# Kernel optimization log

Measured on AMD Instinct MI355X. Metric: run time of the kernel, lower is better.

## Reference

```python
import jax, jax.numpy as jnp
import numpy as np

B, S, D, H = 2, 2048, 1024, 16
HD = D // H
SCALE = HD ** -0.5
EPS = 1e-5


def setup_inputs() -> dict:
    key = jax.random.key(0)
    ks = jax.random.split(key, 12)
    s = 1.0 / np.sqrt(D)
    return {
        "query": jax.random.normal(ks[0], (B, S, D), jnp.float32),
        "key_": jax.random.normal(ks[1], (B, S, D), jnp.float32),
        "value": jax.random.normal(ks[2], (B, S, D), jnp.float32),
        "Wq": jax.random.normal(ks[3], (D, D), jnp.float32) * s,
        "bq": jnp.zeros((D,), jnp.float32),
        "Wk": jax.random.normal(ks[4], (D, D), jnp.float32) * s,
        "bk": jnp.zeros((D,), jnp.float32),
        "Wv": jax.random.normal(ks[5], (D, D), jnp.float32) * s,
        "bv": jnp.zeros((D,), jnp.float32),
        "Wo": jax.random.normal(ks[6], (D, D), jnp.float32) * s,
        "bo": jnp.zeros((D,), jnp.float32),
        "gamma": jnp.ones((D,), jnp.float32),
        "beta": jnp.zeros((D,), jnp.float32),
    }


def _split_heads(x):
    # [B,S,D] -> [B,H,S,HD]
    return x.reshape(B, S, H, HD).transpose(0, 2, 1, 3)


def reference(query, key_, value, Wq, bq, Wk, bk, Wv, bv, Wo, bo, gamma, beta):
    q = _split_heads(query @ Wq + bq)
    k = _split_heads(key_ @ Wk + bk)
    v = _split_heads(value @ Wv + bv)
    # [B,H,S,S] attention scores
    scores = jnp.einsum("bhqd,bhkd->bhqk", q, k) * SCALE
    probs = jax.nn.softmax(scores, axis=-1)  # dropout is identity in eval
    attn = jnp.einsum("bhqk,bhkd->bhqd", probs, v)
    attn = attn.transpose(0, 2, 1, 3).reshape(B, S, D)
    attn = attn @ Wo + bo
    # residual + LayerNorm
    x = query + attn
    mu = jnp.mean(x, axis=-1, keepdims=True)
    var = jnp.mean(jnp.square(x - mu), axis=-1, keepdims=True)
    out = (x - mu) * jax.lax.rsqrt(var + EPS) * gamma + beta
    return out
```

## Files before the change

### kernel.cpp

```cpp
#include <hip/hip_runtime.h>
#include <hip/hip_bf16.h>

#define DEVI __device__ __forceinline__

constexpr int Bb  = 2;
constexpr int Ss  = 2048;
constexpr int Dd  = 1024;
constexpr int Hh  = 16;
constexpr int HDh = 64;
constexpr int Mr  = Bb * Ss;
constexpr float kEps = 1e-5f;
constexpr float kQScale = 0.18033688011112043f;

typedef unsigned short u16;
typedef unsigned int   u32;
typedef u16 u16x8 __attribute__((ext_vector_type(8)));
typedef u16 u16x4 __attribute__((ext_vector_type(4)));
typedef __attribute__((ext_vector_type(8)))  short s16x8;
typedef __attribute__((ext_vector_type(16))) float f32x16;
typedef __attribute__((ext_vector_type(4)))  u32   u32x4;

DEVI float bf2f(u16 u) {
  return __builtin_bit_cast(float, ((unsigned int)u) << 16);
}
DEVI u16 f2bf(float f) {
  unsigned int x = __builtin_bit_cast(unsigned int, f);
  return (u16)((x + 0x7FFFu + ((x >> 16) & 1u)) >> 16);
}
DEVI u32 cvt_pk_bf16(float a, float b) {
  u32 r;
  asm("v_cvt_pk_bf16_f32 %0, %1, %2" : "=v"(r) : "v"(a), "v"(b));
  return r;
}
DEVI float vexp2(float x) {
  float r;
  asm("v_exp_f32 %0, %1" : "=v"(r) : "v"(x));
  return r;
}

DEVI void gload_lds16(const void* g, void* l) {
  __builtin_amdgcn_global_load_lds(
      (const __attribute__((address_space(1))) unsigned int*)(unsigned long long)(size_t)g,
      (__attribute__((address_space(3))) unsigned int*)(unsigned int)(size_t)l,
      16, 0, 0);
}


__global__ __launch_bounds__(256) void pack_a_fm(
    const float* __restrict__ X0, const float* __restrict__ X1,
    u16* __restrict__ Y0, u16* __restrict__ Y1) {
  __shared__ u16 Tl[64 * 64];
  const int t  = threadIdx.x;
  const int k0 = blockIdx.x * 64, r0 = blockIdx.y * 64;
  const float* X = blockIdx.z ? X1 : X0;
  u16*         Y = blockIdx.z ? Y1 : Y0;
#pragma unroll
  for (int i = 0; i < 4; ++i) {
    const int idx = t + i * 256;
    const int r = idx >> 4, c4 = (idx & 15) << 2;
    const float4 v = *(const float4*)(X + (size_t)(r0 + r) * 1024 + k0 + c4);
    u16x4 p;
    p[0] = f2bf(v.x); p[1] = f2bf(v.y); p[2] = f2bf(v.z); p[3] = f2bf(v.w);
    *(u16x4*)&Tl[r * 64 + (c4 ^ (8 * (r & 7)))] = p;
  }
  __syncthreads();
#pragma unroll
  for (int i = 0; i < 2; ++i) {
    const int slot = t + i * 256;
    const int f = slot >> 6, l = slot & 63;
    const int l31 = l & 31, g2 = l >> 5;
    const int r = (f >> 2) * 32 + l31;
    const int c = (f & 3) * 16 + g2 * 8;
    const u16x8 v = *(const u16x8*)&Tl[r * 64 + (c ^ (8 * (r & 7)))];
    const size_t t32 = (size_t)(r0 >> 5) + (f >> 2);
    const int s = (k0 >> 4) + (f & 3);
    *(u16x8*)(Y + (t32 * 64 + s) * 512 + l * 8) = v;
  }
}

__global__ __launch_bounds__(256) void pack_w_fm(
    const float* __restrict__ W0, const float* __restrict__ W1,
    const float* __restrict__ W2, const float* __restrict__ W3,
    u16* __restrict__ WfmBase) {
  __shared__ u16 Tl[64 * 64];
  const int t  = threadIdx.x;
  const int k0 = blockIdx.x * 64, n0 = blockIdx.y * 64;
  const int z  = blockIdx.z;
  const float* W = z == 0 ? W0 : z == 1 ? W1 : z == 2 ? W2 : W3;
  u16* out = WfmBase + (size_t)z * 1024 * 1024;
#pragma unroll
  for (int i = 0; i < 4; ++i) {
    const int idx = t + i * 256;
    const int r = idx >> 4, c4 = (idx & 15) << 2;
    const float4 v = *(const float4*)(W + (size_t)(k0 + r) * 1024 + n0 + c4);
    u16x4 p;
    p[0] = f2bf(v.x); p[1] = f2bf(v.y); p[2] = f2bf(v.z); p[3] = f2bf(v.w);
    *(u16x4*)&Tl[r * 64 + (c4 ^ (8 * (r & 7)))] = p;
  }
  __syncthreads();
#pragma unroll
  for (int i = 0; i < 2; ++i) {
    const int slot = t + i * 256;
    const int f = slot >> 6, l = slot & 63;
    const int l31 = l & 31, g2 = l >> 5;
    const int rbase = (f & 3) * 16 + g2 * 8;
    const int c = (f >> 2) * 32 + l31;
    u16x8 o;
#pragma unroll
    for (int j = 0; j < 8; ++j) {
      const int r = rbase + j;
      o[j] = Tl[r * 64 + (((c & ~3) ^ (8 * (r & 7))) | (c & 3))];
    }
    const size_t n32 = (size_t)(n0 >> 5) + (f >> 2);
    const int s = (k0 >> 4) + (f & 3);
    *(u16x8*)(out + (n32 * 64 + s) * 512 + l * 8) = o;
  }
}

template <int MODE>
__global__ __launch_bounds__(256, 2) void gemm_reg_k(
    const u16* __restrict__ A0, const u16* __restrict__ A1,
    const u16* __restrict__ Wt0, const u16* __restrict__ Wt1,
    const float* b0, const float* b1, void* C0, void* C1,
    float e0, float e1) {
  constexpr int K = 1024, N = 1024;
  const int z = blockIdx.z;
  const u16*   A    = z ? A1 : A0;
  const u16*   Wt   = z ? Wt1 : Wt0;
  const float* bias = z ? b1 : b0;
  void*        Cv   = z ? C1 : C0;
  const float  esc  = z ? e1 : e0;

  const int t = threadIdx.x;
  const int lane = t & 63, w = t >> 6;
  const int l31 = lane & 31, g2 = lane >> 5;
  const int id  = blockIdx.y * 8 + blockIdx.x;
  const int sid = (id & 7) * 32 + (id >> 3);
  const int m0 = (sid >> 3) * 128, n0 = (sid & 7) * 128;
  const int wr = w >> 1, wc = w & 1;

  const u16* a0p = A  + ((size_t)(m0 >> 5) + 2 * wr) * 32768 + lane * 8;
  const u16* a1p = a0p + 32768;
  const u16* w0p = Wt + ((size_t)(n0 >> 5) + 2 * wc) * 32768 + lane * 8;
  const u16* w1p = w0p + 32768;

  f32x16 acc00, acc01, acc10, acc11;
#pragma unroll
  for (int r = 0; r < 16; ++r) { acc00[r] = 0.f; acc01[r] = 0.f; acc10[r] = 0.f; acc11[r] = 0.f; }

  s16x8 X[8], Y[8], Z[8];
  auto loadset = [&](s16x8* R, int k0) {
    const int o = (k0 >> 4) * 512;
    R[0] = *(const s16x8*)(a0p + o);  R[1] = *(const s16x8*)(a0p + o + 512);
    R[2] = *(const s16x8*)(a1p + o);  R[3] = *(const s16x8*)(a1p + o + 512);
    R[4] = *(const s16x8*)(w0p + o);  R[5] = *(const s16x8*)(w0p + o + 512);
    R[6] = *(const s16x8*)(w1p + o);  R[7] = *(const s16x8*)(w1p + o + 512);
  };
  auto compute = [&](const s16x8* R) {
#pragma unroll
    for (int s = 0; s < 2; ++s) {
      if constexpr (MODE == 1) {
        acc00 = __builtin_amdgcn_mfma_f32_32x32x16_bf16(R[0 + s], R[4 + s], acc00, 0, 0, 0);
        acc01 = __builtin_amdgcn_mfma_f32_32x32x16_bf16(R[0 + s], R[6 + s], acc01, 0, 0, 0);
        acc10 = __builtin_amdgcn_mfma_f32_32x32x16_bf16(R[2 + s], R[4 + s], acc10, 0, 0, 0);
        acc11 = __builtin_amdgcn_mfma_f32_32x32x16_bf16(R[2 + s], R[6 + s], acc11, 0, 0, 0);
      } else {
        acc00 = __builtin_amdgcn_mfma_f32_32x32x16_bf16(R[4 + s], R[0 + s], acc00, 0, 0, 0);
        acc01 = __builtin_amdgcn_mfma_f32_32x32x16_bf16(R[4 + s], R[2 + s], acc01, 0, 0, 0);
        acc10 = __builtin_amdgcn_mfma_f32_32x32x16_bf16(R[6 + s], R[0 + s], acc10, 0, 0, 0);
        acc11 = __builtin_amdgcn_mfma_f32_32x32x16_bf16(R[6 + s], R[2 + s], acc11, 0, 0, 0);
      }
    }
  };

  loadset(X, 0); loadset(Y, 32); loadset(Z, 64);
  int k = 0;
  for (int it = 0; it < 9; ++it, k += 96) {
    compute(X); loadset(X, k + 96);
    compute(Y); loadset(Y, k + 128);
    compute(Z); loadset(Z, k + 160);
  }
  compute(X); loadset(X, 960);
  compute(Y); loadset(Y, 992);
  compute(Z);
  compute(X);
  compute(Y);

  if constexpr (MODE == 1) {
    auto storeV = [&](const f32x16& a, int i, int j) {
      const int n = n0 + (2 * wc + j) * 32 + l31;
      const float bn = bias[n];
      u16* vout = (u16*)Cv + ((size_t)(m0 >> 11)) * (1024 * 2048) + (size_t)n * 2048 +
                  (m0 & 2047) + (2 * wr + i) * 32;
#pragma unroll
      for (int c = 0; c < 4; ++c) {
        u16x4 o;
#pragma unroll
        for (int rr = 0; rr < 4; ++rr) o[rr] = f2bf(a[4 * c + rr] + bn);
        *(u16x4*)(vout + 8 * c + 4 * g2) = o;
      }
    };
    storeV(acc00, 0, 0); storeV(acc01, 0, 1); storeV(acc10, 1, 0); storeV(acc11, 1, 1);
  } else {
    auto storeNM = [&](const f32x16& a, int i, int j) {
      const int m = m0 + (2 * wr + j) * 32 + l31;
#pragma unroll
      for (int c = 0; c < 4; ++c) {
        const int nb = n0 + (2 * wc + i) * 32 + 8 * c + 4 * g2;
        const float4 b4 = *(const float4*)&bias[nb];
        if constexpr (MODE == 2) {
          float4 v;
          v.x = a[4 * c + 0] + b4.x; v.y = a[4 * c + 1] + b4.y;
          v.z = a[4 * c + 2] + b4.z; v.w = a[4 * c + 3] + b4.w;
          *(float4*)((float*)Cv + (size_t)m * N + nb) = v;
        } else {
          u16x4 o;
          o[0] = f2bf((a[4 * c + 0] + b4.x) * esc); o[1] = f2bf((a[4 * c + 1] + b4.y) * esc);
          o[2] = f2bf((a[4 * c + 2] + b4.z) * esc); o[3] = f2bf((a[4 * c + 3] + b4.w) * esc);
          *(u16x4*)((u16*)Cv + (size_t)m * N + nb) = o;
        }
      }
    };
    storeNM(acc00, 0, 0); storeNM(acc01, 0, 1); storeNM(acc10, 1, 0); storeNM(acc11, 1, 1);
  }
}

__global__ __launch_bounds__(256) void flash_mfma_k(
    const u16* __restrict__ Qb, const u16* __restrict__ Kb,
    const u16* __restrict__ Vtg, u16* __restrict__ Ofm) {
  __shared__ u16 smem[16384];
  const int t    = threadIdx.x;
  const int lane = t & 63;
  const int w    = t >> 6;
  const int l31  = lane & 31, g2 = lane >> 5;
  const int hid = (blockIdx.z * 16 + blockIdx.y) * 16 + blockIdx.x;
  const int sid = (hid & 7) * 64 + (hid >> 3);
  const int h = (sid >> 4) & 15, b = sid >> 8;
  const int q0 = (sid & 15) * 128 + w * 32;

  s16x8 qf0, qf1, qf2, qf3;
  {
    const u16* qp = Qb + ((size_t)(b * Ss + q0 + l31)) * Dd + h * HDh + 8 * g2;
    qf0 = *(const s16x8*)(qp);
    qf1 = *(const s16x8*)(qp + 16);
    qf2 = *(const s16x8*)(qp + 32);
    qf3 = *(const s16x8*)(qp + 48);
  }

  f32x16 accO0, accO1, zacc;
#pragma unroll
  for (int r = 0; r < 16; ++r) { accO0[r] = 0.f; accO1[r] = 0.f; zacc[r] = 0.f; }
  float l_run = 0.f;

  const int f0 = 2 * w, f1 = 2 * w + 1;
  const u16* kg0 = Kb + ((size_t)(b * Ss + 32 * (f0 >> 2) + l31)) * Dd + h * HDh + 16 * (f0 & 3) + 8 * g2;
  const u16* kg1 = Kb + ((size_t)(b * Ss + 32 * (f1 >> 2) + l31)) * Dd + h * HDh + 16 * (f1 & 3) + 8 * g2;
  const u16* vg0 = Vtg + ((size_t)((b * Hh + h) * HDh + 32 * (f0 >> 2) + l31)) * Ss + 16 * (f0 & 3) + 8 * g2;
  const u16* vg1 = Vtg + ((size_t)((b * Hh + h) * HDh + 32 * (f1 >> 2) + l31)) * Ss + 16 * (f1 & 3) + 8 * g2;

  auto stage = [&](int buf, int kt) {
    u16* base = &smem[buf * 8192];
    gload_lds16(kg0 + (size_t)kt * 64 * Dd, base + f0 * 512);
    gload_lds16(kg1 + (size_t)kt * 64 * Dd, base + f1 * 512);
    gload_lds16(vg0 + kt * 64, base + 4096 + f0 * 512);
    gload_lds16(vg1 + kt * 64, base + 4096 + f1 * 512);
  };

  stage(0, 0);
  __syncthreads();

  int cur = 0;
  for (int kt = 0; kt < Ss / 64; ++kt) {
    if (kt + 1 < Ss / 64) stage(cur ^ 1, kt + 1);
    const u16* sb = &smem[cur * 8192];
    const int lb = lane * 8;

    f32x16 sc0, sc1;
    __builtin_amdgcn_s_setprio(1);
    {
      s16x8 ka, kb2;
      ka  = *(const s16x8*)&sb[(0 * 4 + 0) * 512 + lb];
      kb2 = *(const s16x8*)&sb[(1 * 4 + 0) * 512 + lb];
      sc0 = __builtin_amdgcn_mfma_f32_32x32x16_bf16(ka, qf0, zacc, 0, 0, 0);
      sc1 = __builtin_amdgcn_mfma_f32_32x32x16_bf16(kb2, qf0, zacc, 0, 0, 0);
      ka  = *(const s16x8*)&sb[(0 * 4 + 1) * 512 + lb];
      kb2 = *(const s16x8*)&sb[(1 * 4 + 1) * 512 + lb];
      sc0 = __builtin_amdgcn_mfma_f32_32x32x16_bf16(ka, qf1, sc0, 0, 0, 0);
      sc1 = __builtin_amdgcn_mfma_f32_32x32x16_bf16(kb2, qf1, sc1, 0, 0, 0);
      ka  = *(const s16x8*)&sb[(0 * 4 + 2) * 512 + lb];
      kb2 = *(const s16x8*)&sb[(1 * 4 + 2) * 512 + lb];
      sc0 = __builtin_amdgcn_mfma_f32_32x32x16_bf16(ka, qf2, sc0, 0, 0, 0);
      sc1 = __builtin_amdgcn_mfma_f32_32x32x16_bf16(kb2, qf2, sc1, 0, 0, 0);
      ka  = *(const s16x8*)&sb[(0 * 4 + 3) * 512 + lb];
      kb2 = *(const s16x8*)&sb[(1 * 4 + 3) * 512 + lb];
      sc0 = __builtin_amdgcn_mfma_f32_32x32x16_bf16(ka, qf3, sc0, 0, 0, 0);
      sc1 = __builtin_amdgcn_mfma_f32_32x32x16_bf16(kb2, qf3, sc1, 0, 0, 0);
    }
    __builtin_amdgcn_s_setprio(0);

    float p0[16], p1[16];
    float lp = 0.f;
#pragma unroll
    for (int r = 0; r < 16; ++r) { const float e = vexp2(sc0[r]); p0[r] = e; lp += e; }
#pragma unroll
    for (int r = 0; r < 16; ++r) { const float e = vexp2(sc1[r]); p1[r] = e; lp += e; }
    lp += __shfl_xor(lp, 32);
    l_run += lp;

    u32 pw0[4][2], pw1[4][2];
#pragma unroll
    for (int c = 0; c < 4; ++c) {
      pw0[c][0] = cvt_pk_bf16(p0[4 * c + 0], p0[4 * c + 1]);
      pw0[c][1] = cvt_pk_bf16(p0[4 * c + 2], p0[4 * c + 3]);
      pw1[c][0] = cvt_pk_bf16(p1[4 * c + 0], p1[4 * c + 1]);
      pw1[c][1] = cvt_pk_bf16(p1[4 * c + 2], p1[4 * c + 3]);
    }

#pragma unroll
    for (int s = 0; s < 4; ++s) {
      const int cb = 2 * (s & 1);
      u32 A0w, B0w, A1w, B1w;
      if (s < 2) { A0w = pw0[cb][0]; B0w = pw0[cb + 1][0]; A1w = pw0[cb][1]; B1w = pw0[cb + 1][1]; }
      else       { A0w = pw1[cb][0]; B0w = pw1[cb + 1][0]; A1w = pw1[cb][1]; B1w = pw1[cb + 1][1]; }
      asm("v_permlane32_swap_b32 %0, %1" : "+v"(A0w), "+v"(B0w));
      asm("v_permlane32_swap_b32 %0, %1" : "+v"(A1w), "+v"(B1w));
      u32x4 pv;
      pv[0] = A0w; pv[1] = A1w; pv[2] = B0w; pv[3] = B1w;
      const s16x8 pf = __builtin_bit_cast(s16x8, pv);
      const s16x8 v0 = *(const s16x8*)&sb[4096 + (0 * 4 + s) * 512 + lb];
      const s16x8 v1 = *(const s16x8*)&sb[4096 + (1 * 4 + s) * 512 + lb];
      __builtin_amdgcn_s_setprio(1);
      accO0 = __builtin_amdgcn_mfma_f32_32x32x16_bf16(v0, pf, accO0, 0, 0, 0);
      accO1 = __builtin_amdgcn_mfma_f32_32x32x16_bf16(v1, pf, accO1, 0, 0, 0);
      __builtin_amdgcn_s_setprio(0);
    }
    __syncthreads();
    cur ^= 1;
  }

  const float inv = 1.f / l_run;
  u16* Ol = &smem[w * 2304];
#pragma unroll
  for (int c = 0; c < 4; ++c) {
    u16x4 pk;
#pragma unroll
    for (int rr = 0; rr < 4; ++rr) pk[rr] = f2bf(accO0[4 * c + rr] * inv);
    *(u16x4*)&Ol[l31 * 72 + 0 * 32 + c * 8 + g2 * 4] = pk;
#pragma unroll
    for (int rr = 0; rr < 4; ++rr) pk[rr] = f2bf(accO1[4 * c + rr] * inv);
    *(u16x4*)&Ol[l31 * 72 + 1 * 32 + c * 8 + g2 * 4] = pk;
  }
  const size_t m32 = (size_t)((b * Ss + q0) >> 5);
#pragma unroll
  for (int s = 0; s < 4; ++s) {
    const u16x8 vv = *(const u16x8*)&Ol[l31 * 72 + s * 16 + g2 * 8];
    *(u16x8*)(Ofm + (m32 * 64 + h * 4 + s) * 512 + lane * 8) = vv;
  }
}

__global__ __launch_bounds__(256) void resid_ln_k(const float* __restrict__ x0,
                                                  const float* __restrict__ x1,
                                                  const float* __restrict__ gamma,
                                                  const float* __restrict__ beta,
                                                  float* __restrict__ out) {
  const int row = blockIdx.x;
  const int t   = threadIdx.x;
  const size_t base = (size_t)row * Dd + t * 4;
  const float4 a = *(const float4*)(x0 + base);
  const float4 c = *(const float4*)(x1 + base);
  float x[4] = {a.x + c.x, a.y + c.y, a.z + c.z, a.w + c.w};
  float s  = (x[0] + x[1]) + (x[2] + x[3]);
  float s2 = fmaf(x[0], x[0], fmaf(x[1], x[1], fmaf(x[2], x[2], x[3] * x[3])));
#pragma unroll
  for (int m = 1; m < 64; m <<= 1) {
    s  += __shfl_xor(s, m);
    s2 += __shfl_xor(s2, m);
  }
  __shared__ float red[8];
  const int wave = t >> 6;
  if ((t & 63) == 0) {
    red[wave]     = s;
    red[wave + 4] = s2;
  }
  __syncthreads();
  s  = (red[0] + red[1]) + (red[2] + red[3]);
  s2 = (red[4] + red[5]) + (red[6] + red[7]);
  const float mu  = s * (1.f / Dd);
  const float var = s2 * (1.f / Dd) - mu * mu;
  const float rs  = rsqrtf(var + kEps);
  const float4 g  = *(const float4*)(gamma + t * 4);
  const float4 be = *(const float4*)(beta + t * 4);
  float4 o;
  o.x = (x[0] - mu) * rs * g.x + be.x;
  o.y = (x[1] - mu) * rs * g.y + be.y;
  o.z = (x[2] - mu) * rs * g.z + be.z;
  o.w = (x[3] - mu) * rs * g.w + be.w;
  *(float4*)(out + base) = o;
}

extern "C" void kernel_launch(void* const* d_in, const int* in_sizes, int n_in,
                              void* d_out, int out_size, void* d_ws,
                              size_t ws_size, hipStream_t stream) {
  const float* query = (const float*)d_in[0];
  const float* key_  = (const float*)d_in[1];
  const float* value = (const float*)d_in[2];
  const float* Wq = (const float*)d_in[3];
  const float* bq = (const float*)d_in[4];
  const float* Wk = (const float*)d_in[5];
  const float* bk = (const float*)d_in[6];
  const float* Wv = (const float*)d_in[7];
  const float* bv = (const float*)d_in[8];
  const float* Wo = (const float*)d_in[9];
  const float* bo = (const float*)d_in[10];
  const float* gamma = (const float*)d_in[11];
  const float* beta  = (const float*)d_in[12];
  float* out = (float*)d_out;

  char* ws = (char*)d_ws;
  u16* Qb  = (u16*)(ws + (size_t)0);
  u16* Kb  = (u16*)(ws + (size_t)8 * 1024 * 1024);
  u16* Vtg = (u16*)(ws + (size_t)16 * 1024 * 1024);
  u16* WfB = (u16*)(ws + (size_t)24 * 1024 * 1024);
  u16* Wqf = WfB;
  u16* Wkf = WfB + (size_t)1 * 1024 * 1024;
  u16* Wvf = WfB + (size_t)2 * 1024 * 1024;
  u16* Wof = WfB + (size_t)3 * 1024 * 1024;
  float* Xo = (float*)(ws + (size_t)8 * 1024 * 1024);
  u16* Xv  = (u16*)d_out;
  u16* Xq  = (u16*)d_out;
  u16* Xk  = (u16*)d_out + (size_t)Mr * Dd;
  u16* Ofm = (u16*)d_out;

  pack_a_fm<<<dim3(16, 64, 1), 256, 0, stream>>>(value, value, Xv, Xv);
  pack_w_fm<<<dim3(16, 16, 4), 256, 0, stream>>>(Wq, Wk, Wv, Wo, WfB);
  gemm_reg_k<1><<<dim3(8, 32, 1), 256, 0, stream>>>(
      Xv, Xv, Wvf, Wvf, bv, bv, Vtg, Vtg, 1.f, 1.f);
  pack_a_fm<<<dim3(16, 64, 2), 256, 0, stream>>>(query, key_, Xq, Xk);
  gemm_reg_k<0><<<dim3(8, 32, 2), 256, 0, stream>>>(
      Xq, Xk, Wqf, Wkf, bq, bk, Qb, Kb, kQScale, 1.f);
  flash_mfma_k<<<dim3(16, 16, 2), 256, 0, stream>>>(Qb, Kb, Vtg, Ofm);
  gemm_reg_k<2><<<dim3(8, 32, 1), 256, 0, stream>>>(
      Ofm, Ofm, Wof, Wof, bo, bo, Xo, Xo, 1.f, 1.f);
  resid_ln_k<<<Mr, 256, 0, stream>>>(query, Xo, gamma, beta, out);
}
```

Measured before the change: 140.7 us.

## Split attention KV range in two halves and combine partial outputs

The flash attention grid is doubled so each block processes half of the key/value sequence, and each block writes unnormalised bf16 partial outputs plus its row sums. A new combine kernel adds the two partials and divides by the total row sum before the output projection. This raises the number of attention blocks to improve occupancy and load balance across CUs. In exchange it adds an extra kernel launch, extra global memory traffic for the partials, and some precision loss from rounding the unnormalised partials to bf16.

```diff
diff --git a/kernel.cpp b/kernel.cpp
--- a/kernel.cpp
+++ b/kernel.cpp
@@ -227,16 +227,20 @@
 
 __global__ __launch_bounds__(256) void flash_mfma_k(
     const u16* __restrict__ Qb, const u16* __restrict__ Kb,
-    const u16* __restrict__ Vtg, u16* __restrict__ Ofm) {
+    const u16* __restrict__ Vtg, u16* __restrict__ Opart,
+    float* __restrict__ Lpart) {
   __shared__ u16 smem[16384];
   const int t    = threadIdx.x;
   const int lane = t & 63;
   const int w    = t >> 6;
   const int l31  = lane & 31, g2 = lane >> 5;
   const int hid = (blockIdx.z * 16 + blockIdx.y) * 16 + blockIdx.x;
-  const int sid = (hid & 7) * 64 + (hid >> 3);
-  const int h = (sid >> 4) & 15, b = sid >> 8;
-  const int q0 = (sid & 15) * 128 + w * 32;
+  const int sid = (hid & 7) * 128 + (hid >> 3);
+  const int half = sid & 1;
+  const int q0   = ((sid >> 1) & 15) * 128 + w * 32;
+  const int h    = (sid >> 5) & 15;
+  const int b    = sid >> 9;
+  const int kt0  = half * 16;
 
   s16x8 qf0, qf1, qf2, qf3;
   {
@@ -266,12 +270,13 @@
     gload_lds16(vg1 + kt * 64, base + 4096 + f1 * 512);
   };
 
-  stage(0, 0);
+  stage(0, kt0);
   __syncthreads();
 
   int cur = 0;
-  for (int kt = 0; kt < Ss / 64; ++kt) {
-    if (kt + 1 < Ss / 64) stage(cur ^ 1, kt + 1);
+  for (int i = 0; i < 16; ++i) {
+    const int kt = kt0 + i;
+    if (i + 1 < 16) stage(cur ^ 1, kt + 1);
     const u16* sb = &smem[cur * 8192];
     const int lb = lane * 8;
 
@@ -338,24 +343,47 @@
     cur ^= 1;
   }
 
-  const float inv = 1.f / l_run;
   u16* Ol = &smem[w * 2304];
 #pragma unroll
   for (int c = 0; c < 4; ++c) {
     u16x4 pk;
 #pragma unroll
-    for (int rr = 0; rr < 4; ++rr) pk[rr] = f2bf(accO0[4 * c + rr] * inv);
+    for (int rr = 0; rr < 4; ++rr) pk[rr] = f2bf(accO0[4 * c + rr]);
     *(u16x4*)&Ol[l31 * 72 + 0 * 32 + c * 8 + g2 * 4] = pk;
 #pragma unroll
-    for (int rr = 0; rr < 4; ++rr) pk[rr] = f2bf(accO1[4 * c + rr] * inv);
+    for (int rr = 0; rr < 4; ++rr) pk[rr] = f2bf(accO1[4 * c + rr]);
     *(u16x4*)&Ol[l31 * 72 + 1 * 32 + c * 8 + g2 * 4] = pk;
   }
   const size_t m32 = (size_t)((b * Ss + q0) >> 5);
+  u16* Op = Opart + (size_t)half * 4 * 1024 * 1024;
 #pragma unroll
   for (int s = 0; s < 4; ++s) {
     const u16x8 vv = *(const u16x8*)&Ol[l31 * 72 + s * 16 + g2 * 8];
-    *(u16x8*)(Ofm + (m32 * 64 + h * 4 + s) * 512 + lane * 8) = vv;
-  }
+    *(u16x8*)(Op + (m32 * 64 + h * 4 + s) * 512 + lane * 8) = vv;
+  }
+  if (g2 == 0)
+    Lpart[(size_t)half * 65536 + (((b << 4) + h) << 11) + q0 + l31] = l_run;
+}
+
+__global__ __launch_bounds__(256) void combine_o_k(
+    u16* __restrict__ Oa, const u16* __restrict__ Ob,
+    const float* __restrict__ Lp) {
+  const size_t idx = (size_t)blockIdx.x * 256 + threadIdx.x;
+  const size_t off = idx * 8;
+  const int frag = (int)(off >> 9);
+  const int lane = (int)(off >> 3) & 63;
+  const int row  = (frag >> 6) * 32 + (lane & 31);
+  const int h    = (frag >> 2) & 15;
+  const size_t li = (size_t)(((row >> 11) << 4) + h) * 2048 + (row & 2047);
+  const float inv = 1.f / (Lp[li] + Lp[65536 + li]);
+  const u16x8 a = *(const u16x8*)(Oa + off);
+  const u16x8 b = *(const u16x8*)(Ob + off);
+  u32x4 o;
+#pragma unroll
+  for (int j = 0; j < 4; ++j)
+    o[j] = cvt_pk_bf16((bf2f(a[2 * j]) + bf2f(b[2 * j])) * inv,
+                       (bf2f(a[2 * j + 1]) + bf2f(b[2 * j + 1])) * inv);
+  *(u32x4*)(Oa + off) = o;
 }
 
 __global__ __launch_bounds__(256) void resid_ln_k(const float* __restrict__ x0,
@@ -425,11 +453,13 @@
   u16* Wkf = WfB + (size_t)1 * 1024 * 1024;
   u16* Wvf = WfB + (size_t)2 * 1024 * 1024;
   u16* Wof = WfB + (size_t)3 * 1024 * 1024;
-  float* Xo = (float*)(ws + (size_t)8 * 1024 * 1024);
+  float* Xo    = (float*)(ws + (size_t)8 * 1024 * 1024);
+  float* Lpart = (float*)(ws + (size_t)24 * 1024 * 1024);
   u16* Xv  = (u16*)d_out;
   u16* Xq  = (u16*)d_out;
   u16* Xk  = (u16*)d_out + (size_t)Mr * Dd;
-  u16* Ofm = (u16*)d_out;
+  u16* Opart = (u16*)d_out;
+  u16* Ofm   = (u16*)d_out;
 
   pack_a_fm<<<dim3(16, 64, 1), 256, 0, stream>>>(value, value, Xv, Xv);
   pack_w_fm<<<dim3(16, 16, 4), 256, 0, stream>>>(Wq, Wk, Wv, Wo, WfB);
@@ -438,7 +468,8 @@
   pack_a_fm<<<dim3(16, 64, 2), 256, 0, stream>>>(query, key_, Xq, Xk);
   gemm_reg_k<0><<<dim3(8, 32, 2), 256, 0, stream>>>(
       Xq, Xk, Wqf, Wkf, bq, bk, Qb, Kb, kQScale, 1.f);
-  flash_mfma_k<<<dim3(16, 16, 2), 256, 0, stream>>>(Qb, Kb, Vtg, Ofm);
+  flash_mfma_k<<<dim3(16, 16, 4), 256, 0, stream>>>(Qb, Kb, Vtg, Opart, Lpart);
+  combine_o_k<<<2048, 256, 0, stream>>>(Ofm, Opart + (size_t)4 * 1024 * 1024, Lpart);
   gemm_reg_k<2><<<dim3(8, 32, 1), 256, 0, stream>>>(
       Ofm, Ofm, Wof, Wof, bo, bo, Xo, Xo, 1.f, 1.f);
   resid_ln_k<<<Mr, 256, 0, stream>>>(query, Xo, gamma, beta, out);
```

After: 146.4 us. +4.0%, slower.

## Triple-buffer K/V tiles and interleave QK and PV MFMA halves in flash loop

Applied to the files above, without the earlier changes.

Moves the flash attention loop from double to triple-buffered LDS staging, with a prefetch distance of two tiles. Each iteration now waits with an explicit vmcnt count and a single raw barrier instead of two __syncthreads. It also splits the score computation into two halves so the exp and bf16 packing of the first half can overlap the MFMAs of the second, and defers the cross-lane sum shuffle to after the loop. The cost is more shared memory per block, which may lower occupancy, and reliance on a hand-coded vmcnt count being correct.

```diff
diff --git a/kernel.cpp b/kernel.cpp
--- a/kernel.cpp
+++ b/kernel.cpp
@@ -228,7 +228,7 @@
 __global__ __launch_bounds__(256) void flash_mfma_k(
     const u16* __restrict__ Qb, const u16* __restrict__ Kb,
     const u16* __restrict__ Vtg, u16* __restrict__ Ofm) {
-  __shared__ u16 smem[16384];
+  __shared__ u16 smem[24576];
   const int t    = threadIdx.x;
   const int lane = t & 63;
   const int w    = t >> 6;
@@ -267,61 +267,65 @@
   };
 
   stage(0, 0);
-  __syncthreads();
-
-  int cur = 0;
-  for (int kt = 0; kt < Ss / 64; ++kt) {
-    if (kt + 1 < Ss / 64) stage(cur ^ 1, kt + 1);
-    const u16* sb = &smem[cur * 8192];
+  stage(1, 1);
+
+  int bi = 0;
+  for (int i = 0; i < 32; ++i) {
+    if (i < 31) asm volatile("s_waitcnt vmcnt(4)" ::: "memory");
+    else        asm volatile("s_waitcnt vmcnt(0)" ::: "memory");
+    __builtin_amdgcn_s_barrier();
+    if (i + 2 < 32) {
+      int sbuf = bi + 2; if (sbuf >= 3) sbuf -= 3;
+      stage(sbuf, i + 2);
+    }
+    const u16* sb = &smem[bi * 8192];
     const int lb = lane * 8;
 
     f32x16 sc0, sc1;
     __builtin_amdgcn_s_setprio(1);
     {
-      s16x8 ka, kb2;
+      s16x8 ka;
       ka  = *(const s16x8*)&sb[(0 * 4 + 0) * 512 + lb];
-      kb2 = *(const s16x8*)&sb[(1 * 4 + 0) * 512 + lb];
       sc0 = __builtin_amdgcn_mfma_f32_32x32x16_bf16(ka, qf0, zacc, 0, 0, 0);
-      sc1 = __builtin_amdgcn_mfma_f32_32x32x16_bf16(kb2, qf0, zacc, 0, 0, 0);
       ka  = *(const s16x8*)&sb[(0 * 4 + 1) * 512 + lb];
-      kb2 = *(const s16x8*)&sb[(1 * 4 + 1) * 512 + lb];
       sc0 = __builtin_amdgcn_mfma_f32_32x32x16_bf16(ka, qf1, sc0, 0, 0, 0);
-      sc1 = __builtin_amdgcn_mfma_f32_32x32x16_bf16(kb2, qf1, sc1, 0, 0, 0);
       ka  = *(const s16x8*)&sb[(0 * 4 + 2) * 512 + lb];
-      kb2 = *(const s16x8*)&sb[(1 * 4 + 2) * 512 + lb];
       sc0 = __builtin_amdgcn_mfma_f32_32x32x16_bf16(ka, qf2, sc0, 0, 0, 0);
-      sc1 = __builtin_amdgcn_mfma_f32_32x32x16_bf16(kb2, qf2, sc1, 0, 0, 0);
       ka  = *(const s16x8*)&sb[(0 * 4 + 3) * 512 + lb];
-      kb2 = *(const s16x8*)&sb[(1 * 4 + 3) * 512 + lb];
       sc0 = __builtin_amdgcn_mfma_f32_32x32x16_bf16(ka, qf3, sc0, 0, 0, 0);
-      sc1 = __builtin_amdgcn_mfma_f32_32x32x16_bf16(kb2, qf3, sc1, 0, 0, 0);
     }
     __builtin_amdgcn_s_setprio(0);
 
-    float p0[16], p1[16];
+    float p0[16];
     float lp = 0.f;
 #pragma unroll
     for (int r = 0; r < 16; ++r) { const float e = vexp2(sc0[r]); p0[r] = e; lp += e; }
-#pragma unroll
-    for (int r = 0; r < 16; ++r) { const float e = vexp2(sc1[r]); p1[r] = e; lp += e; }
-    lp += __shfl_xor(lp, 32);
-    l_run += lp;
-
-    u32 pw0[4][2], pw1[4][2];
+    u32 pw0[4][2];
 #pragma unroll
     for (int c = 0; c < 4; ++c) {
       pw0[c][0] = cvt_pk_bf16(p0[4 * c + 0], p0[4 * c + 1]);
       pw0[c][1] = cvt_pk_bf16(p0[4 * c + 2], p0[4 * c + 3]);
-      pw1[c][0] = cvt_pk_bf16(p1[4 * c + 0], p1[4 * c + 1]);
-      pw1[c][1] = cvt_pk_bf16(p1[4 * c + 2], p1[4 * c + 3]);
-    }
-
-#pragma unroll
-    for (int s = 0; s < 4; ++s) {
+    }
+
+    __builtin_amdgcn_s_setprio(1);
+    {
+      s16x8 kb2;
+      kb2 = *(const s16x8*)&sb[(1 * 4 + 0) * 512 + lb];
+      sc1 = __builtin_amdgcn_mfma_f32_32x32x16_bf16(kb2, qf0, zacc, 0, 0, 0);
+      kb2 = *(const s16x8*)&sb[(1 * 4 + 1) * 512 + lb];
+      sc1 = __builtin_amdgcn_mfma_f32_32x32x16_bf16(kb2, qf1, sc1, 0, 0, 0);
+      kb2 = *(const s16x8*)&sb[(1 * 4 + 2) * 512 + lb];
+      sc1 = __builtin_amdgcn_mfma_f32_32x32x16_bf16(kb2, qf2, sc1, 0, 0, 0);
+      kb2 = *(const s16x8*)&sb[(1 * 4 + 3) * 512 + lb];
+      sc1 = __builtin_amdgcn_mfma_f32_32x32x16_bf16(kb2, qf3, sc1, 0, 0, 0);
+    }
+    __builtin_amdgcn_s_setprio(0);
+
+#pragma unroll
+    for (int s = 0; s < 2; ++s) {
       const int cb = 2 * (s & 1);
-      u32 A0w, B0w, A1w, B1w;
-      if (s < 2) { A0w = pw0[cb][0]; B0w = pw0[cb + 1][0]; A1w = pw0[cb][1]; B1w = pw0[cb + 1][1]; }
-      else       { A0w = pw1[cb][0]; B0w = pw1[cb + 1][0]; A1w = pw1[cb][1]; B1w = pw1[cb + 1][1]; }
+      u32 A0w = pw0[cb][0], B0w = pw0[cb + 1][0];
+      u32 A1w = pw0[cb][1], B1w = pw0[cb + 1][1];
       asm("v_permlane32_swap_b32 %0, %1" : "+v"(A0w), "+v"(B0w));
       asm("v_permlane32_swap_b32 %0, %1" : "+v"(A1w), "+v"(B1w));
       u32x4 pv;
@@ -334,11 +338,43 @@
       accO1 = __builtin_amdgcn_mfma_f32_32x32x16_bf16(v1, pf, accO1, 0, 0, 0);
       __builtin_amdgcn_s_setprio(0);
     }
-    __syncthreads();
-    cur ^= 1;
-  }
-
-  const float inv = 1.f / l_run;
+
+    float p1[16];
+#pragma unroll
+    for (int r = 0; r < 16; ++r) { const float e = vexp2(sc1[r]); p1[r] = e; lp += e; }
+    u32 pw1[4][2];
+#pragma unroll
+    for (int c = 0; c < 4; ++c) {
+      pw1[c][0] = cvt_pk_bf16(p1[4 * c + 0], p1[4 * c + 1]);
+      pw1[c][1] = cvt_pk_bf16(p1[4 * c + 2], p1[4 * c + 3]);
+    }
+    l_run += lp;
+
+#pragma unroll
+    for (int s = 2; s < 4; ++s) {
+      const int cb = 2 * (s & 1);
+      u32 A0w = pw1[cb][0], B0w = pw1[cb + 1][0];
+      u32 A1w = pw1[cb][1], B1w = pw1[cb + 1][1];
+      asm("v_permlane32_swap_b32 %0, %1" : "+v"(A0w), "+v"(B0w));
+      asm("v_permlane32_swap_b32 %0, %1" : "+v"(A1w), "+v"(B1w));
+      u32x4 pv;
+      pv[0] = A0w; pv[1] = A1w; pv[2] = B0w; pv[3] = B1w;
+      const s16x8 pf = __builtin_bit_cast(s16x8, pv);
+      const s16x8 v0 = *(const s16x8*)&sb[4096 + (0 * 4 + s) * 512 + lb];
+      const s16x8 v1 = *(const s16x8*)&sb[4096 + (1 * 4 + s) * 512 + lb];
+      __builtin_amdgcn_s_setprio(1);
+      accO0 = __builtin_amdgcn_mfma_f32_32x32x16_bf16(v0, pf, accO0, 0, 0, 0);
+      accO1 = __builtin_amdgcn_mfma_f32_32x32x16_bf16(v1, pf, accO1, 0, 0, 0);
+      __builtin_amdgcn_s_setprio(0);
+    }
+
+    bi = (bi == 2) ? 0 : bi + 1;
+  }
+
+  __syncthreads();
+
+  const float l_tot = l_run + __shfl_xor(l_run, 32);
+  const float inv = 1.f / l_tot;
   u16* Ol = &smem[w * 2304];
 #pragma unroll
   for (int c = 0; c < 4; ++c) {
```

Result: no change. 139.8 us (-0.7%).
